# Optimization experiments

Hardware: AMD Instinct MI355X
Metric: run time of the kernel (lower is better)

## Reference

```python
import jax, jax.numpy as jnp
import numpy as np

B, S, H, NH = 2, 2048, 1024, 16
HD = H // NH  # head size = 64


def setup_inputs() -> dict:
    key = jax.random.key(0)
    ks = jax.random.split(key, 6)
    x = jax.random.normal(ks[0], (B, S, H), dtype=jnp.float32)
    additive_attention_mask = jnp.zeros((S,), dtype=jnp.float32)
    # nn.Linear params: weight [out, in], bias [out]
    w_qkv = jax.random.normal(ks[1], (3 * H, H), dtype=jnp.float32) / np.sqrt(H)
    b_qkv = jax.random.normal(ks[2], (3 * H,), dtype=jnp.float32) * 0.02
    w_o = jax.random.normal(ks[3], (H, H), dtype=jnp.float32) / np.sqrt(H)
    b_o = jax.random.normal(ks[4], (H,), dtype=jnp.float32) * 0.02
    return {"x": x, "additive_attention_mask": additive_attention_mask,
            "w_qkv": w_qkv, "b_qkv": b_qkv, "w_o": w_o, "b_o": b_o}


def reference(x, additive_attention_mask, w_qkv, b_qkv, w_o, b_o):
    # QKV projection: (B,S,H) @ (H,3H) + (3H,)
    qkv = jnp.einsum('bsh,oh->bso', x, w_qkv) + b_qkv
    q, k, v = qkv[..., :H], qkv[..., H:2 * H], qkv[..., 2 * H:]
    # split heads -> (B, NH, S, HD)
    def heads(t):
        return t.reshape(B, S, NH, HD).transpose(0, 2, 1, 3)
    qh, kh, vh = heads(q), heads(k), heads(v)
    # scores (B, NH, Sq, Sk); mask added BEFORE the 1/sqrt(d) scaling (faithful)
    scores = jnp.einsum('bhqd,bhkd->bhqk', qh, kh)
    scores = scores + additive_attention_mask[None, None, None, :]
    probs = jax.nn.softmax(scores / np.sqrt(HD).astype(np.float32), axis=-1)
    # dropout p=0.0 -> identity
    av = jnp.einsum('bhqk,bhkd->bqhd', probs, vh).reshape(B, S, H)
    return jnp.einsum('bsh,oh->bso', av, w_o) + b_o
```

## Files before the change

### kernel.cpp

```cpp
#include <hip/hip_runtime.h>
#include <cmath>

#define B_  2
#define S_  2048
#define H_  1024
#define NH_ 16
#define HD_ 64

typedef _Float16 half8  __attribute__((ext_vector_type(8)));
typedef __fp16   fp16x2 __attribute__((ext_vector_type(2)));
typedef float    f32x16 __attribute__((ext_vector_type(16)));

#define MFMA32(a, b, c) __builtin_amdgcn_mfma_f32_32x32x16_f16((a), (b), (c), 0, 0, 0)

__device__ __forceinline__ void gl2lds16(const void* g, void* l) {
    __builtin_amdgcn_global_load_lds(
        (const __attribute__((address_space(1))) unsigned int*)g,
        (__attribute__((address_space(3))) unsigned int*)l,
        16, 0, 0);
}

__device__ __forceinline__ unsigned pk16(float a, float b) {
    union { fp16x2 v; unsigned u; } c;
    c.v = __builtin_amdgcn_cvt_pkrtz(a, b);
    return c.u;
}

__global__ __launch_bounds__(256, 4)
void conv_hilo(const float* __restrict__ src, _Float16* __restrict__ dh,
               _Float16* __restrict__ dl, int K)
{
    const int bid = blockIdx.x;
    const int nkt = K >> 6;
    const int rt  = bid / nkt;
    const int kt  = bid % nkt;
    const int tid = threadIdx.x;
    const size_t tb = (size_t)bid * 8192;
#pragma unroll
    for (int p = 0; p < 4; ++p) {
        const int idx = p * 256 + tid;
        const int r   = idx >> 3;
        const int g   = idx & 7;
        const float* s = src + (size_t)(rt * 128 + r) * K + kt * 64 + g * 8;
        const float4 v0 = *reinterpret_cast<const float4*>(s);
        const float4 v1 = *reinterpret_cast<const float4*>(s + 4);
        const float f[8] = {v0.x, v0.y, v0.z, v0.w, v1.x, v1.y, v1.z, v1.w};
        half8 hi, lo;
#pragma unroll
        for (int e = 0; e < 8; ++e) {
            const _Float16 hv = (_Float16)f[e];
            hi[e] = hv;
            lo[e] = (_Float16)(f[e] - (float)hv);
        }
        const int dst = r * 64 + ((g ^ (r & 7)) << 3);
        *reinterpret_cast<half8*>(dh + tb + dst) = hi;
        *reinterpret_cast<half8*>(dl + tb + dst) = lo;
    }
}

template<int QKV>
__global__ __launch_bounds__(256, 2)
void hgemm_split(const _Float16* __restrict__ Ah, const _Float16* __restrict__ Al,
                 const _Float16* __restrict__ Wh, const _Float16* __restrict__ Wl,
                 const float* __restrict__ bias, float* __restrict__ C,
                 float* __restrict__ Qo,
                 _Float16* __restrict__ Kh, _Float16* __restrict__ Kl,
                 _Float16* __restrict__ Vh, _Float16* __restrict__ Vl,
                 int nbm, int nbn, int nkt, int N)
{
    __shared__ __align__(16) unsigned char smem[65536];
    _Float16* sAh = (_Float16*)(smem);
    _Float16* sAl = (_Float16*)(smem + 16384);
    _Float16* sWh = (_Float16*)(smem + 32768);
    _Float16* sWl = (_Float16*)(smem + 49152);

    const int tid  = threadIdx.x;
    const int w    = tid >> 6;
    const int lane = tid & 63;
    const int lr   = lane & 31;
    const int hh   = lane >> 5;
    const int wm   = w >> 1, wn = w & 1;

    const int nwg = nbm * nbn;
    const int cpx = nwg >> 3;
    const int bid = blockIdx.x;
    const int wg  = (bid & 7) * cpx + (bid >> 3);
    const int mt  = wg / nbn, nt = wg % nbn;

    const size_t aBase = (size_t)mt * nkt * 8192;
    const size_t wBase = (size_t)nt * nkt * 8192;

    f32x16 acc[2][2];
#pragma unroll
    for (int mi = 0; mi < 2; ++mi)
#pragma unroll
        for (int ni = 0; ni < 2; ++ni)
#pragma unroll
            for (int r = 0; r < 16; ++r) acc[mi][ni][r] = 0.f;

    for (int kt = 0; kt < nkt; ++kt) {
        __syncthreads();
        {
            const size_t at = aBase + (size_t)kt * 8192;
            const size_t wt = wBase + (size_t)kt * 8192;
#pragma unroll
            for (int c = 0; c < 4; ++c) {
                const int loff = (w * 4 + c) * 512;
                const int goff = loff + lane * 8;
                gl2lds16((const void*)(Ah + at + goff), (void*)(sAh + loff));
                gl2lds16((const void*)(Al + at + goff), (void*)(sAl + loff));
                gl2lds16((const void*)(Wh + wt + goff), (void*)(sWh + loff));
                gl2lds16((const void*)(Wl + wt + goff), (void*)(sWl + loff));
            }
        }
        __syncthreads();

#pragma unroll
        for (int ks = 0; ks < 4; ++ks) {
            const int g = ks * 2 + hh;
            half8 aH[2], aL[2], bH[2], bL[2];
#pragma unroll
            for (int mi = 0; mi < 2; ++mi) {
                const int r   = wm * 64 + mi * 32 + lr;
                const int idx = r * 64 + ((g ^ (r & 7)) << 3);
                aH[mi] = *reinterpret_cast<const half8*>(sAh + idx);
                aL[mi] = *reinterpret_cast<const half8*>(sAl + idx);
            }
#pragma unroll
            for (int ni = 0; ni < 2; ++ni) {
                const int c   = wn * 64 + ni * 32 + lr;
                const int idx = c * 64 + ((g ^ (c & 7)) << 3);
                bH[ni] = *reinterpret_cast<const half8*>(sWh + idx);
                bL[ni] = *reinterpret_cast<const half8*>(sWl + idx);
            }
#pragma unroll
            for (int mi = 0; mi < 2; ++mi)
#pragma unroll
                for (int ni = 0; ni < 2; ++ni) {
                    acc[mi][ni] = MFMA32(aH[mi], bH[ni], acc[mi][ni]);
                    acc[mi][ni] = MFMA32(aH[mi], bL[ni], acc[mi][ni]);
                    acc[mi][ni] = MFMA32(aL[mi], bH[ni], acc[mi][ni]);
                }
        }
    }

    if constexpr (QKV == 0) {
        const int n0 = nt * 128 + wn * 64 + lr;
        float bv[2];
#pragma unroll
        for (int ni = 0; ni < 2; ++ni) bv[ni] = bias[n0 + ni * 32];
#pragma unroll
        for (int mi = 0; mi < 2; ++mi)
#pragma unroll
            for (int ni = 0; ni < 2; ++ni)
#pragma unroll
                for (int r = 0; r < 16; ++r) {
                    const int m = mt * 128 + wm * 64 + mi * 32 +
                                  (r & 3) + 8 * (r >> 2) + 4 * hh;
                    C[(size_t)m * N + n0 + ni * 32] = acc[mi][ni][r] + bv[ni];
                }
    } else {
        float* sC = (float*)smem;
        const int m0  = mt * 128;
        const int b   = m0 >> 11;
        const int kt0 = (m0 & 2047) >> 6;
#pragma unroll
        for (int pass = 0; pass < 2; ++pass) {
            __syncthreads();
            if (wm == pass) {
#pragma unroll
                for (int mi = 0; mi < 2; ++mi)
#pragma unroll
                    for (int ni = 0; ni < 2; ++ni)
#pragma unroll
                        for (int r = 0; r < 16; ++r) {
                            const int ml = mi * 32 + (r & 3) + 8 * (r >> 2) + 4 * hh;
                            sC[ml * 132 + wn * 64 + ni * 32 + lr] = acc[mi][ni][r];
                        }
            }
            __syncthreads();
            const int ktile = kt0 + pass;
            if (nt < 8) {
#pragma unroll
                for (int it = 0; it < 8; ++it) {
                    const int idx = it * 256 + tid;
                    const int row = idx >> 5;
                    const int c4  = (idx & 31) << 2;
                    float4 v = *reinterpret_cast<const float4*>(&sC[row * 132 + c4]);
                    const float4 bv = *reinterpret_cast<const float4*>(bias + nt * 128 + c4);
                    v.x += bv.x; v.y += bv.y; v.z += bv.z; v.w += bv.w;
                    *reinterpret_cast<float4*>(
                        Qo + (size_t)(m0 + pass * 64 + row) * 1024 + nt * 128 + c4) = v;
                }
            } else if (nt < 16) {
#pragma unroll
                for (int it = 0; it < 4; ++it) {
                    const int idx = it * 256 + tid;
                    const int key = idx >> 4;
                    const int g   = idx & 15;
                    const int head = 2 * (nt - 8) + (g >> 3);
                    const int d0   = (g & 7) << 3;
                    float f[8];
#pragma unroll
                    for (int e = 0; e < 8; ++e)
                        f[e] = sC[key * 132 + g * 8 + e] +
                               bias[1024 + (nt - 8) * 128 + g * 8 + e];
                    half8 hi, lo;
#pragma unroll
                    for (int e = 0; e < 8; ++e) {
                        const _Float16 hv = (_Float16)f[e];
                        hi[e] = hv;
                        lo[e] = (_Float16)(f[e] - (float)hv);
                    }
                    const size_t base = ((size_t)(b * 16 + head) * 32 + ktile) * 4096;
                    const size_t dst  = base + key * 64 + (d0 ^ ((key & 7) << 3));
                    *reinterpret_cast<half8*>(Kh + dst) = hi;
                    *reinterpret_cast<half8*>(Kl + dst) = lo;
                }
            } else {
#pragma unroll
                for (int it = 0; it < 4; ++it) {
                    const int idx = it * 256 + tid;
                    const int f   = idx >> 3;
                    const int kg  = idx & 7;
                    const int head = 2 * (nt - 16) + (f >> 6);
                    const int d    = f & 63;
                    const float bv = bias[2048 + (nt - 16) * 128 + f];
                    float fe[8];
#pragma unroll
                    for (int e = 0; e < 8; ++e)
                        fe[e] = sC[(kg * 8 + e) * 132 + f] + bv;
                    half8 hi, lo;
#pragma unroll
                    for (int e = 0; e < 8; ++e) {
                        const _Float16 hv = (_Float16)fe[e];
                        hi[e] = hv;
                        lo[e] = (_Float16)(fe[e] - (float)hv);
                    }
                    const size_t base = ((size_t)(b * 16 + head) * 32 + ktile) * 4096;
                    const size_t dst  = base + d * 64 + ((kg * 8) ^ ((d & 7) << 3));
                    *reinterpret_cast<half8*>(Vh + dst) = hi;
                    *reinterpret_cast<half8*>(Vl + dst) = lo;
                }
            }
        }
    }
}

__global__ __launch_bounds__(256, 2)
void attn_mfma(const float* __restrict__ Q, const float* __restrict__ mask,
               const _Float16* __restrict__ Kh, const _Float16* __restrict__ Kl,
               const _Float16* __restrict__ Vh, const _Float16* __restrict__ Vl,
               _Float16* __restrict__ Avh, _Float16* __restrict__ Avl)
{
    __shared__ __align__(16) unsigned char smem[73728];
    float* sM = (float*)(smem + 65536);
    float* sO = (float*)(smem);

    const int tid  = threadIdx.x;
    const int w    = tid >> 6;
    const int lane = tid & 63;
    const int lq   = lane & 31;
    const int hh   = lane >> 5;

    const int bid = blockIdx.x;
    const int wg  = (bid & 7) * 64 + (bid >> 3);
    const int bh  = wg >> 4;
    const int qb  = wg & 15;
    const int b   = bh >> 4, h = bh & 15;

    {
        const float4* mg = reinterpret_cast<const float4*>(mask);
        float4* ms = reinterpret_cast<float4*>(sM);
        float4 a = mg[tid], c = mg[tid + 256];
        a.x *= 0.125f; a.y *= 0.125f; a.z *= 0.125f; a.w *= 0.125f;
        c.x *= 0.125f; c.y *= 0.125f; c.z *= 0.125f; c.w *= 0.125f;
        ms[tid] = a; ms[tid + 256] = c;
    }

    const int qrow = b * S_ + qb * 128 + w * 32 + lq;
    half8 qh[4], ql[4];
#pragma unroll
    for (int ks = 0; ks < 4; ++ks) {
        const float* qp = Q + (size_t)qrow * 1024 + h * HD_ + ks * 16 + hh * 8;
        const float4 a = *reinterpret_cast<const float4*>(qp);
        const float4 c = *reinterpret_cast<const float4*>(qp + 4);
        float qf[8] = {a.x, a.y, a.z, a.w, c.x, c.y, c.z, c.w};
#pragma unroll
        for (int e = 0; e < 8; ++e) {
            const float sv = qf[e] * 0.125f;
            const _Float16 hv = (_Float16)sv;
            qh[ks][e] = hv;
            ql[ks][e] = (_Float16)(sv - (float)hv);
        }
    }

    const int swz = (lq & 7) << 3;
    int off[2][4];
#pragma unroll
    for (int t2 = 0; t2 < 2; ++t2)
#pragma unroll
        for (int ks = 0; ks < 4; ++ks)
            off[t2][ks] = (t2 * 32 + lq) * 64 + ((ks * 16 + hh * 8) ^ swz);

    f32x16 o0 = {0,0,0,0,0,0,0,0,0,0,0,0,0,0,0,0};
    f32x16 o1 = {0,0,0,0,0,0,0,0,0,0,0,0,0,0,0,0};
    float m_run = -INFINITY, l_run = 0.f;

    const size_t bhbase = (size_t)bh * 32 * 4096;

    {
        const size_t tb = bhbase;
#pragma unroll
        for (int i = 0; i < 2; ++i) {
            const int loff = (w * 2 + i) * 512;
            const int goff = loff + lane * 8;
            _Float16* nb = (_Float16*)smem;
            gl2lds16((const void*)(Kh + tb + goff), (void*)(nb + loff));
            gl2lds16((const void*)(Kl + tb + goff), (void*)(nb + 4096 + loff));
            gl2lds16((const void*)(Vh + tb + goff), (void*)(nb + 8192 + loff));
            gl2lds16((const void*)(Vl + tb + goff), (void*)(nb + 12288 + loff));
        }
    }
    __syncthreads();

    for (int kt = 0; kt < 32; ++kt) {
        _Float16* bb = (_Float16*)(smem + ((kt & 1) << 15));
        if (kt < 31) {
            _Float16* nb = (_Float16*)(smem + (((kt + 1) & 1) << 15));
            const size_t tb = bhbase + (size_t)(kt + 1) * 4096;
#pragma unroll
            for (int i = 0; i < 2; ++i) {
                const int loff = (w * 2 + i) * 512;
                const int goff = loff + lane * 8;
                gl2lds16((const void*)(Kh + tb + goff), (void*)(nb + loff));
                gl2lds16((const void*)(Kl + tb + goff), (void*)(nb + 4096 + loff));
                gl2lds16((const void*)(Vh + tb + goff), (void*)(nb + 8192 + loff));
                gl2lds16((const void*)(Vl + tb + goff), (void*)(nb + 12288 + loff));
            }
        }

        f32x16 st[2];
#pragma unroll
        for (int ktt = 0; ktt < 2; ++ktt) {
            f32x16 acc = {0,0,0,0,0,0,0,0,0,0,0,0,0,0,0,0};
#pragma unroll
            for (int ks = 0; ks < 4; ++ks) {
                const half8 ka = *reinterpret_cast<const half8*>(bb + off[ktt][ks]);
                const half8 kb = *reinterpret_cast<const half8*>(bb + 4096 + off[ktt][ks]);
                acc = MFMA32(ka, qh[ks], acc);
                acc = MFMA32(ka, ql[ks], acc);
                acc = MFMA32(kb, qh[ks], acc);
            }
            st[ktt] = acc;
        }

        float mx = -INFINITY;
#pragma unroll
        for (int ktt = 0; ktt < 2; ++ktt) {
#pragma unroll
            for (int rr = 0; rr < 4; ++rr) {
                const int key0 = kt * 64 + ktt * 32 + rr * 8 + hh * 4;
                const float4 mk = *reinterpret_cast<const float4*>(sM + key0);
                const float mkv[4] = {mk.x, mk.y, mk.z, mk.w};
#pragma unroll
                for (int c = 0; c < 4; ++c) {
                    const int r = rr * 4 + c;
                    const float tv = st[ktt][r] + mkv[c];
                    st[ktt][r] = tv;
                    mx = fmaxf(mx, tv);
                }
            }
        }
        mx = fmaxf(mx, __shfl_xor(mx, 32));

        if (!__all(mx - m_run <= 8.0f)) {
            const float mnew = fmaxf(m_run, mx);
            const float corr = __expf(m_run - mnew);
            m_run = mnew;
            l_run *= corr;
#pragma unroll
            for (int r = 0; r < 16; ++r) { o0[r] *= corr; o1[r] *= corr; }
        }
        float ps = 0.f;
#pragma unroll
        for (int ktt = 0; ktt < 2; ++ktt)
#pragma unroll
            for (int r = 0; r < 16; ++r) {
                const float p = __expf(st[ktt][r] - m_run);
                st[ktt][r] = p;
                ps += p;
            }
        ps += __shfl_xor(ps, 32);
        l_run += ps;

        unsigned wph[2][4][2], wpl[2][4][2];
#pragma unroll
        for (int ktt = 0; ktt < 2; ++ktt)
#pragma unroll
            for (int rr = 0; rr < 4; ++rr)
#pragma unroll
                for (int pp = 0; pp < 2; ++pp) {
                    const float p0 = st[ktt][rr * 4 + pp * 2 + 0];
                    const float p1 = st[ktt][rr * 4 + pp * 2 + 1];
                    union { fp16x2 v; unsigned u; } hw;
                    hw.v = __builtin_amdgcn_cvt_pkrtz(p0, p1);
                    wph[ktt][rr][pp] = hw.u;
                    wpl[ktt][rr][pp] = pk16(p0 - (float)hw.v[0], p1 - (float)hw.v[1]);
                }

#pragma unroll
        for (int ks = 0; ks < 4; ++ks) {
            const int i1 = ks >> 1;
            const int rA = (ks & 1) * 2;
            union { unsigned u[4]; half8 v; } ph, pl;
            {
                const unsigned oA0 = wph[i1][rA + 0][0], oB0 = wph[i1][rA + 0][1];
                const unsigned oA1 = wph[i1][rA + 1][0], oB1 = wph[i1][rA + 1][1];
                const unsigned sA1 = (unsigned)__shfl_xor((int)oA1, 32);
                const unsigned sB1 = (unsigned)__shfl_xor((int)oB1, 32);
                const unsigned sA0 = (unsigned)__shfl_xor((int)oA0, 32);
                const unsigned sB0 = (unsigned)__shfl_xor((int)oB0, 32);
                ph.u[0] = hh ? sA1 : oA0;
                ph.u[1] = hh ? sB1 : oB0;
                ph.u[2] = hh ? oA1 : sA0;
                ph.u[3] = hh ? oB1 : sB0;
            }
            {
                const unsigned oA0 = wpl[i1][rA + 0][0], oB0 = wpl[i1][rA + 0][1];
                const unsigned oA1 = wpl[i1][rA + 1][0], oB1 = wpl[i1][rA + 1][1];
                const unsigned sA1 = (unsigned)__shfl_xor((int)oA1, 32);
                const unsigned sB1 = (unsigned)__shfl_xor((int)oB1, 32);
                const unsigned sA0 = (unsigned)__shfl_xor((int)oA0, 32);
                const unsigned sB0 = (unsigned)__shfl_xor((int)oB0, 32);
                pl.u[0] = hh ? sA1 : oA0;
                pl.u[1] = hh ? sB1 : oB0;
                pl.u[2] = hh ? oA1 : sA0;
                pl.u[3] = hh ? oB1 : sB0;
            }
#pragma unroll
            for (int dt = 0; dt < 2; ++dt) {
                const half8 va = *reinterpret_cast<const half8*>(bb + 8192 + off[dt][ks]);
                const half8 vb = *reinterpret_cast<const half8*>(bb + 12288 + off[dt][ks]);
                if (dt == 0) {
                    o0 = MFMA32(va, ph.v, o0);
                    o0 = MFMA32(va, pl.v, o0);
                    o0 = MFMA32(vb, ph.v, o0);
                } else {
                    o1 = MFMA32(va, ph.v, o1);
                    o1 = MFMA32(va, pl.v, o1);
                    o1 = MFMA32(vb, ph.v, o1);
                }
            }
        }
        __syncthreads();
    }

    const float inv = 1.f / l_run;
#pragma unroll
    for (int dt = 0; dt < 2; ++dt)
#pragma unroll
        for (int r = 0; r < 16; ++r) {
            const int d = dt * 32 + (r & 3) + 8 * (r >> 2) + 4 * hh;
            sO[(w * 32 + lq) * 68 + d] = (dt ? o1[r] : o0[r]) * inv;
        }
    __syncthreads();
    {
        const size_t tb = (((size_t)(b * 16 + qb)) * 16 + h) * 8192;
#pragma unroll
        for (int p = 0; p < 4; ++p) {
            const int idx = p * 256 + tid;
            const int q = idx >> 3, g = idx & 7;
            const float4 v0 = *reinterpret_cast<const float4*>(&sO[q * 68 + g * 8]);
            const float4 v1 = *reinterpret_cast<const float4*>(&sO[q * 68 + g * 8 + 4]);
            const float f[8] = {v0.x, v0.y, v0.z, v0.w, v1.x, v1.y, v1.z, v1.w};
            half8 hi, lo;
#pragma unroll
            for (int e = 0; e < 8; ++e) {
                const _Float16 hv = (_Float16)f[e];
                hi[e] = hv;
                lo[e] = (_Float16)(f[e] - (float)hv);
            }
            const int dst = q * 64 + ((g ^ (q & 7)) << 3);
            *reinterpret_cast<half8*>(Avh + tb + dst) = hi;
            *reinterpret_cast<half8*>(Avl + tb + dst) = lo;
        }
    }
}

extern "C" void kernel_launch(void* const* d_in, const int* in_sizes, int n_in,
                              void* d_out, int out_size, void* d_ws, size_t ws_size,
                              hipStream_t stream)
{
    const float* x     = (const float*)d_in[0];
    const float* mask  = (const float*)d_in[1];
    const float* w_qkv = (const float*)d_in[2];
    const float* b_qkv = (const float*)d_in[3];
    const float* w_o   = (const float*)d_in[4];
    const float* b_o   = (const float*)d_in[5];
    float* out = (float*)d_out;

    char* p = (char*)d_ws;
    float*    Qarr = (float*)p;             p += (size_t)4096 * 1024 * 4;
    _Float16* Kh   = (_Float16*)p;          p += (size_t)32 * 32 * 4096 * 2;
    _Float16* Kl   = (_Float16*)p;          p += (size_t)32 * 32 * 4096 * 2;
    _Float16* Vh   = (_Float16*)p;          p += (size_t)32 * 32 * 4096 * 2;
    _Float16* Vl   = (_Float16*)p;          p += (size_t)32 * 32 * 4096 * 2;
    _Float16* Xh   = (_Float16*)p;          p += (size_t)4096 * 1024 * 2;
    _Float16* Xl   = (_Float16*)p;          p += (size_t)4096 * 1024 * 2;
    _Float16* Wqh  = (_Float16*)p;          p += (size_t)3072 * 1024 * 2;
    _Float16* Wql  = (_Float16*)p;          p += (size_t)3072 * 1024 * 2;
    _Float16* Woh  = (_Float16*)p;          p += (size_t)1024 * 1024 * 2;
    _Float16* Wol  = (_Float16*)p;          p += (size_t)1024 * 1024 * 2;
    _Float16* Avh  = (_Float16*)p;          p += (size_t)4096 * 1024 * 2;
    _Float16* Avl  = (_Float16*)p;          p += (size_t)4096 * 1024 * 2;

    const dim3 blk(256);
    conv_hilo<<<dim3(32 * 16), blk, 0, stream>>>(x,     Xh,  Xl,  1024);
    conv_hilo<<<dim3(24 * 16), blk, 0, stream>>>(w_qkv, Wqh, Wql, 1024);
    conv_hilo<<<dim3(8 * 16),  blk, 0, stream>>>(w_o,   Woh, Wol, 1024);

    hgemm_split<1><<<dim3(32 * 24), blk, 0, stream>>>(
        Xh, Xl, Wqh, Wql, b_qkv, nullptr, Qarr, Kh, Kl, Vh, Vl, 32, 24, 16, 3072);
    attn_mfma<<<dim3(512), blk, 0, stream>>>(Qarr, mask, Kh, Kl, Vh, Vl, Avh, Avl);
    hgemm_split<0><<<dim3(32 * 8), blk, 0, stream>>>(
        Avh, Avl, Woh, Wol, b_o, out, nullptr, nullptr, nullptr, nullptr, nullptr,
        32, 8, 16, 1024);
}
```

Before: 343.1 us.

## Double-buffer GEMM LDS tiles and use exp2 with log2e-folded scaling in attention

The split-fp16 GEMM now uses two 64KB LDS buffers and prefetches the next K-tile while computing the current one, so each iteration needs one barrier instead of two and global-to-LDS loads overlap the MFMAs. Because LDS doubles to 128KB, the launch bound drops to one block per CU. Separately, the attention kernel folds log2(e) into the Q and mask scaling, uses the hardware exp2 instruction instead of __expf, and rescales the lazy-rescale threshold to match. The risk is lower occupancy in the GEMM and small numerical differences from the exp2 path.

```diff
diff --git a/kernel.cpp b/kernel.cpp
--- a/kernel.cpp
+++ b/kernel.cpp
@@ -25,6 +25,18 @@
     c.v = __builtin_amdgcn_cvt_pkrtz(a, b);
     return c.u;
 }
+
+__device__ __forceinline__ float exp2_hw(float x) {
+#if __has_builtin(__builtin_amdgcn_exp2f)
+    return __builtin_amdgcn_exp2f(x);
+#else
+    return __expf(x * 0.6931471805599453f);
+#endif
+}
+
+#define LOG2E   1.4426950408889634f
+#define SCALE_  (0.125f * LOG2E)
+#define THR2_   11.5415603f
 
 __global__ __launch_bounds__(256, 4)
 void conv_hilo(const float* __restrict__ src, _Float16* __restrict__ dh,
@@ -59,7 +71,7 @@
 }
 
 template<int QKV>
-__global__ __launch_bounds__(256, 2)
+__global__ __launch_bounds__(256, 1)
 void hgemm_split(const _Float16* __restrict__ Ah, const _Float16* __restrict__ Al,
                  const _Float16* __restrict__ Wh, const _Float16* __restrict__ Wl,
                  const float* __restrict__ bias, float* __restrict__ C,
@@ -68,11 +80,7 @@
                  _Float16* __restrict__ Vh, _Float16* __restrict__ Vl,
                  int nbm, int nbn, int nkt, int N)
 {
-    __shared__ __align__(16) unsigned char smem[65536];
-    _Float16* sAh = (_Float16*)(smem);
-    _Float16* sAl = (_Float16*)(smem + 16384);
-    _Float16* sWh = (_Float16*)(smem + 32768);
-    _Float16* sWl = (_Float16*)(smem + 49152);
+    __shared__ __align__(16) unsigned char smem[131072];
 
     const int tid  = threadIdx.x;
     const int w    = tid >> 6;
@@ -98,22 +106,32 @@
 #pragma unroll
             for (int r = 0; r < 16; ++r) acc[mi][ni][r] = 0.f;
 
+    auto stage = [&](int kt, int buf) {
+        const size_t at = aBase + (size_t)kt * 8192;
+        const size_t wt = wBase + (size_t)kt * 8192;
+        unsigned char* sb = smem + (buf << 16);
+#pragma unroll
+        for (int c = 0; c < 4; ++c) {
+            const int loff = (w * 4 + c) * 512;
+            const int goff = loff + lane * 8;
+            gl2lds16((const void*)(Ah + at + goff), (void*)((_Float16*)sb + loff));
+            gl2lds16((const void*)(Al + at + goff), (void*)((_Float16*)(sb + 16384) + loff));
+            gl2lds16((const void*)(Wh + wt + goff), (void*)((_Float16*)(sb + 32768) + loff));
+            gl2lds16((const void*)(Wl + wt + goff), (void*)((_Float16*)(sb + 49152) + loff));
+        }
+    };
+
+    stage(0, 0);
+    __syncthreads();
+
     for (int kt = 0; kt < nkt; ++kt) {
-        __syncthreads();
-        {
-            const size_t at = aBase + (size_t)kt * 8192;
-            const size_t wt = wBase + (size_t)kt * 8192;
-#pragma unroll
-            for (int c = 0; c < 4; ++c) {
-                const int loff = (w * 4 + c) * 512;
-                const int goff = loff + lane * 8;
-                gl2lds16((const void*)(Ah + at + goff), (void*)(sAh + loff));
-                gl2lds16((const void*)(Al + at + goff), (void*)(sAl + loff));
-                gl2lds16((const void*)(Wh + wt + goff), (void*)(sWh + loff));
-                gl2lds16((const void*)(Wl + wt + goff), (void*)(sWl + loff));
-            }
-        }
-        __syncthreads();
+        if (kt + 1 < nkt) stage(kt + 1, (kt + 1) & 1);
+
+        unsigned char* sb = smem + ((kt & 1) << 16);
+        _Float16* sAh = (_Float16*)(sb);
+        _Float16* sAl = (_Float16*)(sb + 16384);
+        _Float16* sWh = (_Float16*)(sb + 32768);
+        _Float16* sWl = (_Float16*)(sb + 49152);
 
 #pragma unroll
         for (int ks = 0; ks < 4; ++ks) {
@@ -142,6 +160,7 @@
                     acc[mi][ni] = MFMA32(aL[mi], bH[ni], acc[mi][ni]);
                 }
         }
+        __syncthreads();
     }
 
     if constexpr (QKV == 0) {
@@ -273,8 +292,8 @@
         const float4* mg = reinterpret_cast<const float4*>(mask);
         float4* ms = reinterpret_cast<float4*>(sM);
         float4 a = mg[tid], c = mg[tid + 256];
-        a.x *= 0.125f; a.y *= 0.125f; a.z *= 0.125f; a.w *= 0.125f;
-        c.x *= 0.125f; c.y *= 0.125f; c.z *= 0.125f; c.w *= 0.125f;
+        a.x *= SCALE_; a.y *= SCALE_; a.z *= SCALE_; a.w *= SCALE_;
+        c.x *= SCALE_; c.y *= SCALE_; c.z *= SCALE_; c.w *= SCALE_;
         ms[tid] = a; ms[tid + 256] = c;
     }
 
@@ -288,7 +307,7 @@
         float qf[8] = {a.x, a.y, a.z, a.w, c.x, c.y, c.z, c.w};
 #pragma unroll
         for (int e = 0; e < 8; ++e) {
-            const float sv = qf[e] * 0.125f;
+            const float sv = qf[e] * SCALE_;
             const _Float16 hv = (_Float16)sv;
             qh[ks][e] = hv;
             ql[ks][e] = (_Float16)(sv - (float)hv);
@@ -374,9 +393,9 @@
         }
         mx = fmaxf(mx, __shfl_xor(mx, 32));
 
-        if (!__all(mx - m_run <= 8.0f)) {
+        if (!__all(mx - m_run <= THR2_)) {
             const float mnew = fmaxf(m_run, mx);
-            const float corr = __expf(m_run - mnew);
+            const float corr = exp2_hw(m_run - mnew);
             m_run = mnew;
             l_run *= corr;
 #pragma unroll
@@ -387,7 +406,7 @@
         for (int ktt = 0; ktt < 2; ++ktt)
 #pragma unroll
             for (int r = 0; r < 16; ++r) {
-                const float p = __expf(st[ktt][r] - m_run);
+                const float p = exp2_hw(st[ktt][r] - m_run);
                 st[ktt][r] = p;
                 ps += p;
             }
```

Result: faster. 335.3 us (-2.3%).
